# Optimization experiments

Measured on AMD Instinct MI355X. Metric: run time of the kernel, lower is better.

## Reference

```python
import jax, jax.numpy as jnp
import numpy as np
import math

D_MODEL = 256
D_STATE = 16
D_CONV = 4
EXPAND = 2
N_HEADS = 4
D_INNER = EXPAND * D_MODEL          # 512
DT_RANK = (D_MODEL + 15) // 16      # 16
B_SZ, SEQ = 4, 2048


def setup_inputs() -> dict:
    key = jax.random.key(0)
    ks = jax.random.split(key, 12)
    rn = lambda i, shp, sc=0.02: jax.random.normal(ks[i], shp, dtype=jnp.float32) * sc
    x = jax.random.normal(ks[0], (B_SZ, SEQ, D_MODEL), dtype=jnp.float32)
    return dict(
        x=x,
        ln_g=jnp.ones((D_MODEL,), jnp.float32),
        ln_b=jnp.zeros((D_MODEL,), jnp.float32),
        W_in=rn(1, (D_MODEL, 2 * D_INNER)),
        conv_w=rn(2, (D_INNER, D_CONV), 0.1),
        conv_b=jnp.zeros((D_INNER,), jnp.float32),
        W_xproj=rn(3, (D_INNER, DT_RANK + 2 * D_STATE)),
        W_dt=rn(4, (DT_RANK, D_INNER), 0.1),
        b_dt=jnp.full((D_INNER,), -4.6, jnp.float32),  # softplus ~ 0.01 init
        A_log=jnp.log(jnp.tile(jnp.arange(1, D_STATE + 1, dtype=jnp.float32), (D_INNER, 1))),
        Dp=jnp.ones((D_INNER,), jnp.float32),
        W_out_m=rn(5, (D_INNER, D_MODEL)),
        W_qkv=rn(6, (D_MODEL, 3 * D_MODEL)),
        b_qkv=jnp.zeros((3 * D_MODEL,), jnp.float32),
        W_o=rn(7, (D_MODEL, D_MODEL)),
        b_o=jnp.zeros((D_MODEL,), jnp.float32),
        W_gate=rn(8, (2 * D_MODEL, D_MODEL)),
        b_gate=jnp.zeros((D_MODEL,), jnp.float32),
    )


def _sssd_forward(x, ln_g, ln_b, W_in, conv_w, conv_b, W_xproj, W_dt, b_dt,
                  A_log, Dp, W_out_m, W_qkv, b_qkv, W_o, b_o, W_gate, b_gate):
    B, L, D = x.shape
    # LayerNorm
    mu = x.mean(-1, keepdims=True)
    var = x.var(-1, keepdims=True)
    xn = (x - mu) * jax.lax.rsqrt(var + 1e-5) * ln_g + ln_b

    # ---- Mamba branch ----
    xz = xn @ W_in                      # (B,L,2*D_INNER)
    xm, z = jnp.split(xz, 2, axis=-1)
    # causal depthwise conv1d (kernel D_CONV)
    xp = jnp.pad(xm, ((0, 0), (D_CONV - 1, 0), (0, 0)))
    xc = conv_b + sum(xp[:, k:k + L, :] * conv_w[:, k] for k in range(D_CONV))
    xc = jax.nn.silu(xc)
    dbl = xc @ W_xproj                  # (B,L,DT_RANK+2*D_STATE)
    dt_in = dbl[..., :DT_RANK]
    Bm = dbl[..., DT_RANK:DT_RANK + D_STATE]
    Cm = dbl[..., DT_RANK + D_STATE:]
    dt = jax.nn.softplus(dt_in @ W_dt + b_dt)   # (B,L,D_INNER)
    A = -jnp.exp(A_log)                 # (D_INNER, D_STATE)

    def step(h, inp):
        x_t, dt_t, B_t, C_t = inp       # (B,Din),(B,Din),(B,N),(B,N)
        dA = jnp.exp(dt_t[..., None] * A)               # (B,Din,N)
        h = dA * h + (dt_t * x_t)[..., None] * B_t[:, None, :]
        y = jnp.einsum('bdn,bn->bd', h, C_t)
        return h, y

    h0 = jnp.zeros((B, D_INNER, D_STATE), x.dtype)
    xs = (jnp.swapaxes(xc, 0, 1), jnp.swapaxes(dt, 0, 1),
          jnp.swapaxes(Bm, 0, 1), jnp.swapaxes(Cm, 0, 1))
    _, ys = jax.lax.scan(step, h0, xs)
    y = jnp.swapaxes(ys, 0, 1) + xc * Dp
    y = y * jax.nn.silu(z)
    ssm_out = y @ W_out_m               # (B,L,D)

    # ---- MHSA branch (eval: no dropout) ----
    hd = D // N_HEADS
    qkv = xn @ W_qkv + b_qkv
    q, k, v = jnp.split(qkv, 3, axis=-1)
    sh = lambda t: t.reshape(B, L, N_HEADS, hd).transpose(0, 2, 1, 3)
    q, k, v = sh(q), sh(k), sh(v)
    scores = jnp.einsum('bhqd,bhkd->bhqk', q, k) * (1.0 / math.sqrt(hd))
    attn = jax.nn.softmax(scores, axis=-1)
    o = jnp.einsum('bhqk,bhkd->bhqd', attn, v).transpose(0, 2, 1, 3).reshape(B, L, D)
    attn_out = o @ W_o + b_o

    # ---- sigmoid gate fusion ----
    gate = jax.nn.sigmoid(jnp.concatenate([ssm_out, attn_out], axis=-1) @ W_gate + b_gate)
    fused = gate * ssm_out + (1.0 - gate) * attn_out
    return x + fused


def reference(x, ln_g, ln_b, W_in, conv_w, conv_b, W_xproj, W_dt, b_dt,
              A_log, Dp, W_out_m, W_qkv, b_qkv, W_o, b_o, W_gate, b_gate):
    return _sssd_forward(x, ln_g, ln_b, W_in, conv_w, conv_b, W_xproj, W_dt, b_dt,
                         A_log, Dp, W_out_m, W_qkv, b_qkv, W_o, b_o, W_gate, b_gate)
```

## Files before the change

kernel.cpp:

```cpp
#include <hip/hip_runtime.h>
#include <math.h>

#define B_SZ 4
#define SEQ 2048
#define DM 256
#define DI 512
#define DS 16
#define DTR 16
#define NH 4
#define HD 64
#define T_TOK (B_SZ*SEQ)
#define NCH 64
#define CL (SEQ/NCH)
#define QSCALE 0.18033688f

typedef short bf16x8 __attribute__((ext_vector_type(8)));
typedef float f32x4  __attribute__((ext_vector_type(4)));
typedef float f32x16 __attribute__((ext_vector_type(16)));
typedef unsigned short u16;

__device__ __forceinline__ float sigmoidf_(float x){ return 1.f/(1.f+__expf(-x)); }
__device__ __forceinline__ u16 f2bf(float x){
  unsigned int u = __float_as_uint(x);
  u += 0x7fffu + ((u>>16)&1u);
  return (u16)(u>>16);
}
__device__ __forceinline__ float bf2f(u16 u){ return __uint_as_float(((unsigned)u)<<16); }
__device__ __forceinline__ unsigned cvt_pk_bf16(float lo, float hi){
  unsigned r;
  asm("v_cvt_pk_bf16_f32 %0, %1, %2" : "=v"(r) : "v"(lo), "v"(hi));
  return r;
}
__device__ __forceinline__ void permswap(unsigned &a, unsigned &b){
  asm volatile("v_permlane32_swap_b32 %0, %1" : "+v"(a), "+v"(b));
}
__device__ __forceinline__ float xor32f(float v){
  unsigned a = __float_as_uint(v), b = a;
  permswap(a, b);
  return __uint_as_float(a);
}

struct TcvtArgs {
  const float* src[6];
  u16* dst[6];
  int K[6];
  int Nvalid[6];
  int Npad[6];
};
__global__ __launch_bounds__(256) void tcvt_all(TcvtArgs a) {
  int wi = blockIdx.z;
  int K = a.K[wi], Nv = a.Nvalid[wi], Np = a.Npad[wi];
  int k0 = blockIdx.x*64, n0 = blockIdx.y*64;
  if (k0 >= K || n0 >= Np) return;
  __shared__ u16 tile[64][65];
  const float* src = a.src[wi];
  u16* dst = a.dst[wi];
  int tn = threadIdx.x & 63, tq = threadIdx.x >> 6;
#pragma unroll
  for (int j=0;j<16;++j){
    int kk = j*4 + tq;
    int n = n0 + tn;
    tile[tn][kk] = (n < Nv) ? f2bf(src[(size_t)(k0+kk)*Nv + n]) : (u16)0;
  }
  __syncthreads();
#pragma unroll
  for (int j=0;j<16;++j){
    int nn = j*4 + tq;
    dst[(size_t)(n0+nn)*K + k0 + tn] = tile[nn][tn];
  }
}

__global__ __launch_bounds__(256) void ln_kernel(const float* __restrict__ x,
    const float* __restrict__ g, const float* __restrict__ b,
    u16* __restrict__ xn_bf) {
  int wid = threadIdx.x >> 6;
  int lane = threadIdx.x & 63;
  int token = blockIdx.x*4 + wid;
  const float* xr = x + (size_t)token*DM;
  float4 v = *(const float4*)&xr[lane*4];
  float s  = v.x+v.y+v.z+v.w;
  float ss = v.x*v.x+v.y*v.y+v.z*v.z+v.w*v.w;
  for (int m=1;m<64;m<<=1){ s += __shfl_xor(s,m); ss += __shfl_xor(ss,m); }
  float mu  = s * (1.f/DM);
  float var = ss*(1.f/DM) - mu*mu;
  float rs  = rsqrtf(var + 1e-5f);
  float4 gv = *(const float4*)&g[lane*4];
  float4 bv = *(const float4*)&b[lane*4];
  uint2 o;
  o.x = cvt_pk_bf16((v.x-mu)*rs*gv.x + bv.x, (v.y-mu)*rs*gv.y + bv.y);
  o.y = cvt_pk_bf16((v.z-mu)*rs*gv.z + bv.z, (v.w-mu)*rs*gv.w + bv.w);
  *(uint2*)&xn_bf[(size_t)token*DM + lane*4] = o;
}

template<int ACT>
__global__ __launch_bounds__(256) void gemm_mfma(const u16* __restrict__ A,
    const u16* __restrict__ Wt, const float* __restrict__ bias,
    float* __restrict__ C, u16* __restrict__ Cbf, int K, int ldc, int nvalid,
    int qcols, float qscale, const float* __restrict__ xres,
    const float* __restrict__ cat2, u16* __restrict__ vTout) {
  __shared__ u16 lds[12288];
  int tid = threadIdx.x;
  int m0 = blockIdx.y*128, n0 = blockIdx.x*64;
  int w = tid>>6, l = tid&63, lq = l&15, lg = l>>4;
  int wm = w>>1, wn = w&1;
  f32x4 acc[4][2] = {};
  for (int k0 = 0; k0 < K; k0 += 64) {
#pragma unroll
    for (int i=0;i<4;++i){
      int gid = i*256 + tid;
      int row = gid>>3, g = gid&7;
      *(bf16x8*)&lds[row*64 + ((g ^ (row&7))*8)] =
          *(const bf16x8*)&A[(size_t)(m0+row)*K + k0 + g*8];
    }
#pragma unroll
    for (int i=0;i<2;++i){
      int gid = i*256 + tid;
      int row = gid>>3, g = gid&7;
      *(bf16x8*)&lds[8192 + row*64 + ((g ^ (row&7))*8)] =
          *(const bf16x8*)&Wt[(size_t)(n0+row)*K + k0 + g*8];
    }
    __syncthreads();
#pragma unroll
    for (int ks=0;ks<2;++ks){
      bf16x8 af[4], bfv[2];
#pragma unroll
      for (int mi=0;mi<4;++mi){
        int row = wm*64 + mi*16 + lq;
        af[mi] = *(bf16x8*)&lds[row*64 + (((ks*4+lg) ^ (row&7))*8)];
      }
#pragma unroll
      for (int nj=0;nj<2;++nj){
        int row = wn*32 + nj*16 + lq;
        bfv[nj] = *(bf16x8*)&lds[8192 + row*64 + (((ks*4+lg) ^ (row&7))*8)];
      }
#pragma unroll
      for (int mi=0;mi<4;++mi)
#pragma unroll
        for (int nj=0;nj<2;++nj)
          acc[mi][nj] = __builtin_amdgcn_mfma_f32_16x16x32_bf16(af[mi], bfv[nj], acc[mi][nj], 0,0,0);
    }
    __syncthreads();
  }
#pragma unroll
  for (int mi=0;mi<4;++mi){
#pragma unroll
    for (int nj=0;nj<2;++nj){
#pragma unroll
      for (int r=0;r<4;++r){
        int row = m0 + wm*64 + mi*16 + lg*4 + r;
        int col = n0 + wn*32 + nj*16 + lq;
        if (col < nvalid) {
          float v = acc[mi][nj][r];
          if (bias) v += bias[col];
          if (col < qcols) v *= qscale;
          if (ACT==2) {
            float g = sigmoidf_(v);
            float sv = cat2[(size_t)row*512 + col];
            float av = cat2[(size_t)row*512 + 256 + col];
            C[(size_t)row*256 + col] = xres[(size_t)row*256 + col] + g*sv + (1.f-g)*av;
          } else if (ACT==3) {
            Cbf[(size_t)row*ldc + col] = f2bf(v);
            if (col >= 512) {
              int bb = row>>11, ll = row&2047;
              int hh = (col-512)>>6, dd = (col-512)&63;
              vTout[(((size_t)(bb*4+hh))*64 + dd)*SEQ + ll] = f2bf(v);
            }
          } else {
            if (ACT==1) v = sigmoidf_(v);
            if (C)   C[(size_t)row*ldc + col] = v;
            if (Cbf) Cbf[(size_t)row*ldc + col] = f2bf(v);
          }
        }
      }
    }
  }
}

__global__ __launch_bounds__(256) void conv_kernel(const u16* __restrict__ xzb,
    const float* __restrict__ cw, const float* __restrict__ cb,
    u16* __restrict__ xc_bf) {
  int idx = blockIdx.x*256 + threadIdx.x;
  int d2 = (idx & 255)*2;
  int t = idx >> 8;
  int l = t & (SEQ-1);
  float acc0 = cb[d2], acc1 = cb[d2+1];
  float4 wA = *(const float4*)&cw[d2*4];
  float4 wB = *(const float4*)&cw[d2*4+4];
  const u16* base = xzb + (size_t)t*1024 + d2;
  ushort2 v;
  if (l>=3){ v = *(const ushort2*)&base[-3*1024]; acc0 += bf2f(v.x)*wA.x; acc1 += bf2f(v.y)*wB.x; }
  if (l>=2){ v = *(const ushort2*)&base[-2*1024]; acc0 += bf2f(v.x)*wA.y; acc1 += bf2f(v.y)*wB.y; }
  if (l>=1){ v = *(const ushort2*)&base[-1*1024]; acc0 += bf2f(v.x)*wA.z; acc1 += bf2f(v.y)*wB.z; }
  v = *(const ushort2*)&base[0];
  acc0 += bf2f(v.x)*wA.w; acc1 += bf2f(v.y)*wB.w;
  float r0 = acc0 * sigmoidf_(acc0);
  float r1 = acc1 * sigmoidf_(acc1);
  *(unsigned*)&xc_bf[(size_t)t*DI + d2] = cvt_pk_bf16(r0, r1);
}

__global__ __launch_bounds__(256) void dt_kernel(const float* __restrict__ dbl,
    const float* __restrict__ Wdt, const float* __restrict__ bdt,
    u16* __restrict__ dt) {
  __shared__ float sdbl[4][16];
  int wid = threadIdx.x>>6, lane = threadIdx.x&63;
  int token = blockIdx.x*4 + wid;
  if (lane < 16) sdbl[wid][lane] = dbl[(size_t)token*48 + lane];
  __syncthreads();
  float din[16];
#pragma unroll
  for (int k=0;k<16;++k) din[k] = sdbl[wid][k];
#pragma unroll
  for (int r=0;r<8;++r){
    int d = lane + r*64;
    float acc = bdt[d];
#pragma unroll
    for (int k=0;k<16;++k) acc += din[k]*Wdt[k*DI+d];
    float sp = (acc > 20.f) ? acc : log1pf(__expf(acc));
    dt[(size_t)token*DI+d] = f2bf(sp);
  }
}

__global__ __launch_bounds__(512) void scan_p1(const u16* __restrict__ xc_bf,
    const u16* __restrict__ dt, const float* __restrict__ dbl,
    const float* __restrict__ A_log, u16* __restrict__ Pws, u16* __restrict__ Hws) {
  __shared__ float sB[CL][16];
  int d = threadIdx.x;
  int bc = blockIdx.x;
  int b = bc >> 6, c = bc & 63;
  {
    int t = threadIdx.x >> 4, n = threadIdx.x & 15;
    sB[t][n] = dbl[((size_t)b*SEQ + c*CL + t)*48 + DTR + n];
  }
  __syncthreads();
  float An[16];
#pragma unroll
  for (int i=0;i<4;++i){
    float4 a = *(const float4*)&A_log[d*16 + i*4];
    An[i*4+0] = -__expf(a.x); An[i*4+1] = -__expf(a.y);
    An[i*4+2] = -__expf(a.z); An[i*4+3] = -__expf(a.w);
  }
  float h[16] = {};
  float P[16];
#pragma unroll
  for (int n=0;n<16;++n) P[n] = 1.f;
  size_t tok = (size_t)b*SEQ + c*CL;
  for (int t=0;t<CL;++t,++tok){
    float dtv = bf2f(dt[tok*DI+d]);
    float xcv = bf2f(xc_bf[tok*DI+d]);
    float u = dtv*xcv;
    float4 B0 = *(float4*)&sB[t][0];
    float4 B1 = *(float4*)&sB[t][4];
    float4 B2 = *(float4*)&sB[t][8];
    float4 B3 = *(float4*)&sB[t][12];
    float Bv[16] = {B0.x,B0.y,B0.z,B0.w,B1.x,B1.y,B1.z,B1.w,
                    B2.x,B2.y,B2.z,B2.w,B3.x,B3.y,B3.z,B3.w};
#pragma unroll
    for (int n=0;n<16;++n){
      float e = __expf(dtv*An[n]);
      P[n] *= e;
      h[n] = e*h[n] + u*Bv[n];
    }
  }
  size_t base = (((size_t)b*NCH + c)*DI + d)*16;
#pragma unroll
  for (int i=0;i<8;++i){
    *(unsigned*)&Pws[base + i*2] = cvt_pk_bf16(P[i*2], P[i*2+1]);
    *(unsigned*)&Hws[base + i*2] = cvt_pk_bf16(h[i*2], h[i*2+1]);
  }
}

__global__ __launch_bounds__(256) void scan_combine(const u16* __restrict__ Pws,
    const u16* __restrict__ Hws, u16* __restrict__ H0ws) {
  int gid = blockIdx.x*256 + threadIdx.x;
  int b  = gid >> 13;
  int dn = gid & 8191;
  float h0 = 0.f;
#pragma unroll 4
  for (int c=0;c<NCH;++c){
    size_t idx = ((size_t)(b*NCH+c)<<13) + dn;
    H0ws[idx] = f2bf(h0);
    h0 = bf2f(Pws[idx])*h0 + bf2f(Hws[idx]);
  }
}

__global__ __launch_bounds__(512) void scan_p2(const u16* __restrict__ xc_bf,
    const u16* __restrict__ dt, const float* __restrict__ dbl,
    const float* __restrict__ A_log, const float* __restrict__ Dp,
    const u16* __restrict__ xzb, const u16* __restrict__ H0ws,
    u16* __restrict__ ygate_bf) {
  __shared__ float sBC[CL][32];
  int d = threadIdx.x;
  int bc = blockIdx.x;
  int b = bc >> 6, c = bc & 63;
#pragma unroll
  for (int i=0;i<2;++i){
    int idx = i*512 + threadIdx.x;
    int t = idx >> 5, q = idx & 31;
    sBC[t][q] = dbl[((size_t)b*SEQ + c*CL + t)*48 + DTR + q];
  }
  __syncthreads();
  float An[16];
#pragma unroll
  for (int i=0;i<4;++i){
    float4 a = *(const float4*)&A_log[d*16 + i*4];
    An[i*4+0] = -__expf(a.x); An[i*4+1] = -__expf(a.y);
    An[i*4+2] = -__expf(a.z); An[i*4+3] = -__expf(a.w);
  }
  float Dd = Dp[d];
  float h[16];
  size_t base = (((size_t)b*NCH + c)*DI + d)*16;
  {
    bf16x8 h8a = *(const bf16x8*)&H0ws[base];
    bf16x8 h8b = *(const bf16x8*)&H0ws[base+8];
#pragma unroll
    for (int n=0;n<8;++n){ h[n] = bf2f((u16)h8a[n]); h[8+n] = bf2f((u16)h8b[n]); }
  }
  size_t tok = (size_t)b*SEQ + c*CL;
  for (int t=0;t<CL;++t,++tok){
    float dtv = bf2f(dt[tok*DI+d]);
    float xcv = bf2f(xc_bf[tok*DI+d]);
    float zv  = bf2f(xzb[tok*1024 + DI + d]);
    float u = dtv*xcv;
    float4 B0 = *(float4*)&sBC[t][0];
    float4 B1 = *(float4*)&sBC[t][4];
    float4 B2 = *(float4*)&sBC[t][8];
    float4 B3 = *(float4*)&sBC[t][12];
    float4 C0 = *(float4*)&sBC[t][16];
    float4 C1 = *(float4*)&sBC[t][20];
    float4 C2 = *(float4*)&sBC[t][24];
    float4 C3 = *(float4*)&sBC[t][28];
    float Bv[16] = {B0.x,B0.y,B0.z,B0.w,B1.x,B1.y,B1.z,B1.w,
                    B2.x,B2.y,B2.z,B2.w,B3.x,B3.y,B3.z,B3.w};
    float Cv[16] = {C0.x,C0.y,C0.z,C0.w,C1.x,C1.y,C1.z,C1.w,
                    C2.x,C2.y,C2.z,C2.w,C3.x,C3.y,C3.z,C3.w};
    float y = 0.f;
#pragma unroll
    for (int n=0;n<16;++n){
      float e = __expf(dtv*An[n]);
      h[n] = e*h[n] + u*Bv[n];
      y += h[n]*Cv[n];
    }
    y += xcv*Dd;
    ygate_bf[tok*DI + d] = f2bf(y * (zv*sigmoidf_(zv)));
  }
}

__global__ __launch_bounds__(256) void attn_mfma_kernel(const u16* __restrict__ qkvb,
    const u16* __restrict__ vT,
    u16* __restrict__ Opart, float* __restrict__ ml) {
  __shared__ u16 lds[8192];
  int H = blockIdx.x + 8*blockIdx.y + 128*(int)blockIdx.z;
  int cx = H & 7, kk = H >> 3;
  int xq = kk & 7;
  int G  = cx*8 + (kk >> 3);
  int bh = G & 15, s = G >> 4;
  int b = bh>>2, h = bh&3;
  int tid = threadIdx.x;
  int w = tid>>6, l = tid&63;
  int lo32 = l & 31;
  int hi = l >> 5;
  size_t bbase = (size_t)b*SEQ;
  size_t vbase = (size_t)bh*HD*SEQ;
  int q_base = xq*256 + w*64;

  bf16x8 qf[2][4];
#pragma unroll
  for (int qg=0; qg<2; ++qg)
#pragma unroll
    for (int dsl=0; dsl<4; ++dsl)
      qf[qg][dsl] = *(const bf16x8*)&qkvb[(bbase + q_base + qg*32 + lo32)*768 + h*HD + dsl*16 + hi*8];

  float m_[2] = {-1e30f,-1e30f}, l_[2] = {0.f,0.f};
  f32x16 oacc[2][2] = {};

  int srow = tid>>3, sg = tid&7;
  int kt0 = s*8;
  bf16x8 kreg[2], vreg[2];

#define LOADT(kt) { \
  kreg[0] = *(const bf16x8*)&qkvb[(bbase + (size_t)(kt)*64 + srow)*768 + 256 + h*HD + sg*8]; \
  kreg[1] = *(const bf16x8*)&qkvb[(bbase + (size_t)(kt)*64 + srow + 32)*768 + 256 + h*HD + sg*8]; \
  vreg[0] = *(const bf16x8*)&vT[vbase + (size_t)srow*SEQ + (kt)*64 + sg*8]; \
  vreg[1] = *(const bf16x8*)&vT[vbase + (size_t)(srow+32)*SEQ + (kt)*64 + sg*8]; }
#define STORET() { \
  *(bf16x8*)&lds[srow*64 + ((sg ^ (srow&7))*8)] = kreg[0]; \
  *(bf16x8*)&lds[(srow+32)*64 + ((sg ^ ((srow+32)&7))*8)] = kreg[1]; \
  *(bf16x8*)&lds[4096 + srow*64 + ((sg ^ (srow&7))*8)] = vreg[0]; \
  *(bf16x8*)&lds[4096 + (srow+32)*64 + ((sg ^ ((srow+32)&7))*8)] = vreg[1]; }
#define EXCH(X, Y, s_own, s_oth) { \
  unsigned xa = (X), yb = (Y); \
  permswap(xa, yb); \
  s_own = (l < 32) ? (X) : xa; \
  s_oth = (l < 32) ? yb : (Y); }

  LOADT(kt0);
  for (int it=0; it<8; ++it){
    __syncthreads();
    STORET();
    __syncthreads();
    if (it < 7) LOADT(kt0+it+1);

#pragma unroll
    for (int t32=0; t32<2; ++t32){
      int krow = t32*32 + lo32;
      bf16x8 kf[4];
#pragma unroll
      for (int dsl=0; dsl<4; ++dsl)
        kf[dsl] = *(bf16x8*)&lds[krow*64 + (((dsl*2 + hi) ^ (krow&7))*8)];

      bf16x8 pf[2][2];
#pragma unroll
      for (int qg=0; qg<2; ++qg){
        f32x16 sacc = {0,0,0,0,0,0,0,0,0,0,0,0,0,0,0,0};
#pragma unroll
        for (int dsl=0; dsl<4; ++dsl)
          sacc = __builtin_amdgcn_mfma_f32_32x32x16_bf16(kf[dsl], qf[qg][dsl], sacc, 0,0,0);

        float tm = sacc[0];
#pragma unroll
        for (int r=1;r<16;++r) tm = fmaxf(tm, sacc[r]);
        tm = fmaxf(tm, xor32f(tm));
        if (__any(tm - m_[qg] > 8.f)) {
          float mn = fmaxf(m_[qg], tm);
          float sc = exp2f(m_[qg] - mn);
          m_[qg] = mn;
          l_[qg] *= sc;
#pragma unroll
          for (int r=0;r<16;++r){ oacc[qg][0][r] *= sc; oacc[qg][1][r] *= sc; }
        }
        float p[16];
        float ps = 0.f;
#pragma unroll
        for (int r=0;r<16;++r){ p[r] = exp2f(sacc[r] - m_[qg]); ps += p[r]; }
        ps += xor32f(ps);
        l_[qg] += ps;

        unsigned A0 = cvt_pk_bf16(p[0],p[1]),  A1 = cvt_pk_bf16(p[2],p[3]);
        unsigned B0 = cvt_pk_bf16(p[4],p[5]),  B1 = cvt_pk_bf16(p[6],p[7]);
        unsigned C0 = cvt_pk_bf16(p[8],p[9]),  C1 = cvt_pk_bf16(p[10],p[11]);
        unsigned D0 = cvt_pk_bf16(p[12],p[13]),D1 = cvt_pk_bf16(p[14],p[15]);
        unsigned s0,s1,s2,s3,s4,s5,s6,s7;
        EXCH(A0,B0,s0,s2); EXCH(A1,B1,s1,s3);
        EXCH(C0,D0,s4,s6); EXCH(C1,D1,s5,s7);
        ((unsigned*)&pf[qg][0])[0]=s0; ((unsigned*)&pf[qg][0])[1]=s1;
        ((unsigned*)&pf[qg][0])[2]=s2; ((unsigned*)&pf[qg][0])[3]=s3;
        ((unsigned*)&pf[qg][1])[0]=s4; ((unsigned*)&pf[qg][1])[1]=s5;
        ((unsigned*)&pf[qg][1])[2]=s6; ((unsigned*)&pf[qg][1])[3]=s7;
      }

#pragma unroll
      for (int dtile=0; dtile<2; ++dtile){
        int vrow = dtile*32 + lo32;
        bf16x8 vf0 = *(bf16x8*)&lds[4096 + vrow*64 + (((t32*4 + 0 + hi) ^ (vrow&7))*8)];
        bf16x8 vf1 = *(bf16x8*)&lds[4096 + vrow*64 + (((t32*4 + 2 + hi) ^ (vrow&7))*8)];
        oacc[0][dtile] = __builtin_amdgcn_mfma_f32_32x32x16_bf16(vf0, pf[0][0], oacc[0][dtile], 0,0,0);
        oacc[0][dtile] = __builtin_amdgcn_mfma_f32_32x32x16_bf16(vf1, pf[0][1], oacc[0][dtile], 0,0,0);
        oacc[1][dtile] = __builtin_amdgcn_mfma_f32_32x32x16_bf16(vf0, pf[1][0], oacc[1][dtile], 0,0,0);
        oacc[1][dtile] = __builtin_amdgcn_mfma_f32_32x32x16_bf16(vf1, pf[1][1], oacc[1][dtile], 0,0,0);
      }
    }
  }
#undef LOADT
#undef STORET
#undef EXCH

  int sidx = bh*4 + s;
#pragma unroll
  for (int qg=0; qg<2; ++qg){
    size_t rb = ((size_t)sidx*SEQ + q_base + qg*32 + lo32)*64;
#pragma unroll
    for (int dtile=0; dtile<2; ++dtile){
#pragma unroll
      for (int rg=0; rg<4; ++rg){
        uint2 pk;
        pk.x = cvt_pk_bf16(oacc[qg][dtile][rg*4+0], oacc[qg][dtile][rg*4+1]);
        pk.y = cvt_pk_bf16(oacc[qg][dtile][rg*4+2], oacc[qg][dtile][rg*4+3]);
        *(uint2*)&Opart[rb + dtile*32 + rg*8 + 4*hi] = pk;
      }
    }
    if (l < 32){
      ml[((size_t)sidx*SEQ + q_base + qg*32 + lo32)*2    ] = m_[qg];
      ml[((size_t)sidx*SEQ + q_base + qg*32 + lo32)*2 + 1] = l_[qg];
    }
  }
}

__global__ __launch_bounds__(256) void attn_merge_kernel(const u16* __restrict__ Opart,
    const float* __restrict__ ml, u16* __restrict__ attn_bf) {
  int w = threadIdx.x>>6, lane = threadIdx.x&63;
  int R = blockIdx.x*4 + w;
  int bh = R>>11, q = R&2047;
  float m[4], lv[4];
#pragma unroll
  for (int s=0;s<4;++s){
    m[s]  = ml[((size_t)(bh*4+s)*SEQ + q)*2];
    lv[s] = ml[((size_t)(bh*4+s)*SEQ + q)*2 + 1];
  }
  float ms = fmaxf(fmaxf(m[0],m[1]),fmaxf(m[2],m[3]));
  float o = 0.f, lsum = 0.f;
#pragma unroll
  for (int s=0;s<4;++s){
    float wsc = exp2f(m[s]-ms);
    lsum += wsc*lv[s];
    o += wsc*bf2f(Opart[((size_t)(bh*4+s)*SEQ + q)*64 + lane]);
  }
  size_t token = (size_t)(bh>>2)*SEQ + q;
  attn_bf[token*DM + (bh&3)*HD + lane] = f2bf(o/lsum);
}

extern "C" void kernel_launch(void* const* d_in, const int* in_sizes, int n_in,
                              void* d_out, int out_size, void* d_ws, size_t ws_size,
                              hipStream_t stream) {
  const float* x      = (const float*)d_in[0];
  const float* ln_g   = (const float*)d_in[1];
  const float* ln_b   = (const float*)d_in[2];
  const float* W_in   = (const float*)d_in[3];
  const float* conv_w = (const float*)d_in[4];
  const float* conv_b = (const float*)d_in[5];
  const float* W_xproj= (const float*)d_in[6];
  const float* W_dt   = (const float*)d_in[7];
  const float* b_dt   = (const float*)d_in[8];
  const float* A_log  = (const float*)d_in[9];
  const float* Dp     = (const float*)d_in[10];
  const float* W_out_m= (const float*)d_in[11];
  const float* W_qkv  = (const float*)d_in[12];
  const float* b_qkv  = (const float*)d_in[13];
  const float* W_o    = (const float*)d_in[14];
  const float* b_o    = (const float*)d_in[15];
  const float* W_gate = (const float*)d_in[16];
  const float* b_gate = (const float*)d_in[17];
  float* out = (float*)d_out;

  float* ws = (float*)d_ws;
  u16*   xn_bf   = (u16*)(ws);
  u16*   xzb     = (u16*)(ws + 1048576);
  u16*   qkv_bf  = (u16*)(ws + 9437184);
  u16*   xc_bf   = (u16*)(ws + 12582912);
  float* dblb    = ws + 16777216;
  u16*   dtb     = (u16*)(ws + 17170432);
  u16*   ygate_bf= (u16*)(ws + 21364736);
  u16*   attn_bf = (u16*)(ws + 23461888);
  float* catb    = ws + 24510464;
  u16*   catb_bf = (u16*)(ws + 28704768);
  float* gateb   = ws + 30801920;
  u16*   Wt_all  = (u16*)(ws + 32899072);
  u16*   Opart = (u16*)(ws + 1048576);
  float* mlb   = (float*)xn_bf;
  u16*   vTb   = (u16*)gateb;
  u16*   Pws   = (u16*)catb;
  u16*   Hws   = (u16*)(catb + 1048576);
  u16*   H0ws  = (u16*)(catb + 2097152);

  u16* Wt_in   = Wt_all;
  u16* Wt_qkv  = Wt_all + 262144;
  u16* Wt_out  = Wt_all + 458752;
  u16* Wt_o    = Wt_all + 589824;
  u16* Wt_gate = Wt_all + 655360;
  u16* Wt_xp   = Wt_all + 786432;

  TcvtArgs ta;
  ta.src[0]=W_in;    ta.dst[0]=Wt_in;   ta.K[0]=256; ta.Nvalid[0]=1024; ta.Npad[0]=1024;
  ta.src[1]=W_qkv;   ta.dst[1]=Wt_qkv;  ta.K[1]=256; ta.Nvalid[1]=768;  ta.Npad[1]=768;
  ta.src[2]=W_out_m; ta.dst[2]=Wt_out;  ta.K[2]=512; ta.Nvalid[2]=256;  ta.Npad[2]=256;
  ta.src[3]=W_o;     ta.dst[3]=Wt_o;    ta.K[3]=256; ta.Nvalid[3]=256;  ta.Npad[3]=256;
  ta.src[4]=W_gate;  ta.dst[4]=Wt_gate; ta.K[4]=512; ta.Nvalid[4]=256;  ta.Npad[4]=256;
  ta.src[5]=W_xproj; ta.dst[5]=Wt_xp;   ta.K[5]=512; ta.Nvalid[5]=48;   ta.Npad[5]=64;
  tcvt_all<<<dim3(8,16,6), 256, 0, stream>>>(ta);

  ln_kernel<<<T_TOK/4, 256, 0, stream>>>(x, ln_g, ln_b, xn_bf);
  gemm_mfma<0><<<dim3(16,64), 256, 0, stream>>>(xn_bf, Wt_in, nullptr, nullptr, xzb, 256, 1024, 1024, 0, 1.f, nullptr, nullptr, nullptr);
  gemm_mfma<3><<<dim3(12,64), 256, 0, stream>>>(xn_bf, Wt_qkv, b_qkv, nullptr, qkv_bf, 256, 768, 768, 256, QSCALE, nullptr, nullptr, vTb);
  conv_kernel<<<T_TOK, 256, 0, stream>>>(xzb, conv_w, conv_b, xc_bf);
  gemm_mfma<0><<<dim3(1,64), 256, 0, stream>>>(xc_bf, Wt_xp, nullptr, dblb, nullptr, 512, 48, 48, 0, 1.f, nullptr, nullptr, nullptr);
  dt_kernel<<<T_TOK/4, 256, 0, stream>>>(dblb, W_dt, b_dt, dtb);
  scan_p1<<<B_SZ*NCH, 512, 0, stream>>>(xc_bf, dtb, dblb, A_log, Pws, Hws);
  scan_combine<<<128, 256, 0, stream>>>(Pws, Hws, H0ws);
  scan_p2<<<B_SZ*NCH, 512, 0, stream>>>(xc_bf, dtb, dblb, A_log, Dp, xzb, H0ws, ygate_bf);
  attn_mfma_kernel<<<dim3(8, 16, 4), 256, 0, stream>>>(qkv_bf, vTb, Opart, mlb);
  attn_merge_kernel<<<8192, 256, 0, stream>>>(Opart, mlb, attn_bf);
  gemm_mfma<0><<<dim3(4,64), 256, 0, stream>>>(ygate_bf, Wt_out, nullptr, catb, catb_bf, 512, 512, 256, 0, 1.f, nullptr, nullptr, nullptr);
  gemm_mfma<0><<<dim3(4,64), 256, 0, stream>>>(attn_bf, Wt_o, b_o, catb+256, catb_bf+256, 256, 512, 256, 0, 1.f, nullptr, nullptr, nullptr);
  gemm_mfma<2><<<dim3(4,64), 256, 0, stream>>>(catb_bf, Wt_gate, b_gate, out, nullptr, 512, 256, 256, 0, 1.f, x, catb, nullptr);
}
```

Measured before the change: 242.6 us.

## Fuse dt projection into scan passes and attention merge into Wo GEMM

Removes the separate dt_kernel and computes the dt projection plus softplus inline inside both scan passes, using the dt_in columns staged in shared memory. The dt intermediate buffer and its global round trip go away, but each pass now recomputes a 16-term dot product and a log1p/exp per element. The attention split-K merge kernel is also folded into the A-tile load of the output-projection GEMM through a new ACT==4 path. That path reads the four partial outputs and their max/sum stats directly, so attn_bf is no longer materialised. The price is extra ALU work in the serial scan loop and heavier, less coalesced loads in the GEMM prologue.

```diff
diff --git a/kernel.cpp b/kernel.cpp
--- a/kernel.cpp
+++ b/kernel.cpp
@@ -97,7 +97,8 @@
     const u16* __restrict__ Wt, const float* __restrict__ bias,
     float* __restrict__ C, u16* __restrict__ Cbf, int K, int ldc, int nvalid,
     int qcols, float qscale, const float* __restrict__ xres,
-    const float* __restrict__ cat2, u16* __restrict__ vTout) {
+    const float* __restrict__ cat2, u16* __restrict__ vTout,
+    const float* __restrict__ mlp) {
   __shared__ u16 lds[12288];
   int tid = threadIdx.x;
   int m0 = blockIdx.y*128, n0 = blockIdx.x*64;
@@ -105,12 +106,49 @@
   int wm = w>>1, wn = w&1;
   f32x4 acc[4][2] = {};
   for (int k0 = 0; k0 < K; k0 += 64) {
-#pragma unroll
-    for (int i=0;i<4;++i){
-      int gid = i*256 + tid;
-      int row = gid>>3, g = gid&7;
-      *(bf16x8*)&lds[row*64 + ((g ^ (row&7))*8)] =
-          *(const bf16x8*)&A[(size_t)(m0+row)*K + k0 + g*8];
+    if (ACT==4) {
+#pragma unroll
+      for (int i=0;i<4;++i){
+        int gid = i*256 + tid;
+        int row = gid>>3, g = gid&7;
+        int token = m0+row;
+        int bq = token>>11, q = token&2047;
+        int dcol = k0 + g*8;
+        int hh = dcol>>6, dd = dcol&63;
+        int bh4 = (bq*4+hh)*4;
+        float mm[4], lv[4];
+#pragma unroll
+        for (int s4=0;s4<4;++s4){
+          mm[s4] = mlp[((size_t)(bh4+s4)*SEQ+q)*2];
+          lv[s4] = mlp[((size_t)(bh4+s4)*SEQ+q)*2+1];
+        }
+        float ms = fmaxf(fmaxf(mm[0],mm[1]),fmaxf(mm[2],mm[3]));
+        float wsc[4]; float lsum=0.f;
+#pragma unroll
+        for (int s4=0;s4<4;++s4){ wsc[s4]=exp2f(mm[s4]-ms); lsum += wsc[s4]*lv[s4]; }
+        float inv = 1.f/lsum;
+        bf16x8 vpart[4];
+#pragma unroll
+        for (int s4=0;s4<4;++s4)
+          vpart[s4] = *(const bf16x8*)&A[(((size_t)(bh4+s4)*SEQ)+q)*64 + dd];
+        bf16x8 outv;
+#pragma unroll
+        for (int j=0;j<8;++j){
+          float o = 0.f;
+#pragma unroll
+          for (int s4=0;s4<4;++s4) o += wsc[s4]*bf2f((u16)vpart[s4][j]);
+          outv[j] = (short)f2bf(o*inv);
+        }
+        *(bf16x8*)&lds[row*64 + ((g ^ (row&7))*8)] = outv;
+      }
+    } else {
+#pragma unroll
+      for (int i=0;i<4;++i){
+        int gid = i*256 + tid;
+        int row = gid>>3, g = gid&7;
+        *(bf16x8*)&lds[row*64 + ((g ^ (row&7))*8)] =
+            *(const bf16x8*)&A[(size_t)(m0+row)*K + k0 + g*8];
+      }
     }
 #pragma unroll
     for (int i=0;i<2;++i){
@@ -198,40 +236,25 @@
   *(unsigned*)&xc_bf[(size_t)t*DI + d2] = cvt_pk_bf16(r0, r1);
 }
 
-__global__ __launch_bounds__(256) void dt_kernel(const float* __restrict__ dbl,
+__global__ __launch_bounds__(512) void scan_p1(const u16* __restrict__ xc_bf,
+    const float* __restrict__ dbl, const float* __restrict__ A_log,
     const float* __restrict__ Wdt, const float* __restrict__ bdt,
-    u16* __restrict__ dt) {
-  __shared__ float sdbl[4][16];
-  int wid = threadIdx.x>>6, lane = threadIdx.x&63;
-  int token = blockIdx.x*4 + wid;
-  if (lane < 16) sdbl[wid][lane] = dbl[(size_t)token*48 + lane];
-  __syncthreads();
-  float din[16];
-#pragma unroll
-  for (int k=0;k<16;++k) din[k] = sdbl[wid][k];
-#pragma unroll
-  for (int r=0;r<8;++r){
-    int d = lane + r*64;
-    float acc = bdt[d];
-#pragma unroll
-    for (int k=0;k<16;++k) acc += din[k]*Wdt[k*DI+d];
-    float sp = (acc > 20.f) ? acc : log1pf(__expf(acc));
-    dt[(size_t)token*DI+d] = f2bf(sp);
-  }
-}
-
-__global__ __launch_bounds__(512) void scan_p1(const u16* __restrict__ xc_bf,
-    const u16* __restrict__ dt, const float* __restrict__ dbl,
-    const float* __restrict__ A_log, u16* __restrict__ Pws, u16* __restrict__ Hws) {
-  __shared__ float sB[CL][16];
+    u16* __restrict__ Pws, u16* __restrict__ Hws) {
+  __shared__ float sB[CL][32];
   int d = threadIdx.x;
   int bc = blockIdx.x;
   int b = bc >> 6, c = bc & 63;
   {
     int t = threadIdx.x >> 4, n = threadIdx.x & 15;
-    sB[t][n] = dbl[((size_t)b*SEQ + c*CL + t)*48 + DTR + n];
+#pragma unroll
+    for (int i=0;i<2;++i)
+      sB[t][i*16+n] = dbl[((size_t)b*SEQ + c*CL + t)*48 + i*16 + n];
   }
   __syncthreads();
+  float wdt[16];
+#pragma unroll
+  for (int k=0;k<16;++k) wdt[k] = Wdt[k*DI + d];
+  float bdt_d = bdt[d];
   float An[16];
 #pragma unroll
   for (int i=0;i<4;++i){
@@ -245,13 +268,16 @@
   for (int n=0;n<16;++n) P[n] = 1.f;
   size_t tok = (size_t)b*SEQ + c*CL;
   for (int t=0;t<CL;++t,++tok){
-    float dtv = bf2f(dt[tok*DI+d]);
+    float dacc = bdt_d;
+#pragma unroll
+    for (int k=0;k<16;++k) dacc += sB[t][k]*wdt[k];
+    float dtv = (dacc > 20.f) ? dacc : log1pf(__expf(dacc));
     float xcv = bf2f(xc_bf[tok*DI+d]);
     float u = dtv*xcv;
-    float4 B0 = *(float4*)&sB[t][0];
-    float4 B1 = *(float4*)&sB[t][4];
-    float4 B2 = *(float4*)&sB[t][8];
-    float4 B3 = *(float4*)&sB[t][12];
+    float4 B0 = *(float4*)&sB[t][16];
+    float4 B1 = *(float4*)&sB[t][20];
+    float4 B2 = *(float4*)&sB[t][24];
+    float4 B3 = *(float4*)&sB[t][28];
     float Bv[16] = {B0.x,B0.y,B0.z,B0.w,B1.x,B1.y,B1.z,B1.w,
                     B2.x,B2.y,B2.z,B2.w,B3.x,B3.y,B3.z,B3.w};
 #pragma unroll
@@ -284,21 +310,25 @@
 }
 
 __global__ __launch_bounds__(512) void scan_p2(const u16* __restrict__ xc_bf,
-    const u16* __restrict__ dt, const float* __restrict__ dbl,
-    const float* __restrict__ A_log, const float* __restrict__ Dp,
-    const u16* __restrict__ xzb, const u16* __restrict__ H0ws,
-    u16* __restrict__ ygate_bf) {
-  __shared__ float sBC[CL][32];
+    const float* __restrict__ dbl, const float* __restrict__ A_log,
+    const float* __restrict__ Wdt, const float* __restrict__ bdt,
+    const float* __restrict__ Dp, const u16* __restrict__ xzb,
+    const u16* __restrict__ H0ws, u16* __restrict__ ygate_bf) {
+  __shared__ float sBC[CL][48];
   int d = threadIdx.x;
   int bc = blockIdx.x;
   int b = bc >> 6, c = bc & 63;
-#pragma unroll
-  for (int i=0;i<2;++i){
-    int idx = i*512 + threadIdx.x;
-    int t = idx >> 5, q = idx & 31;
-    sBC[t][q] = dbl[((size_t)b*SEQ + c*CL + t)*48 + DTR + q];
+  {
+    int t = threadIdx.x >> 4, n = threadIdx.x & 15;
+#pragma unroll
+    for (int i=0;i<3;++i)
+      sBC[t][i*16+n] = dbl[((size_t)b*SEQ + c*CL + t)*48 + i*16 + n];
   }
   __syncthreads();
+  float wdt[16];
+#pragma unroll
+  for (int k=0;k<16;++k) wdt[k] = Wdt[k*DI + d];
+  float bdt_d = bdt[d];
   float An[16];
 #pragma unroll
   for (int i=0;i<4;++i){
@@ -317,18 +347,21 @@
   }
   size_t tok = (size_t)b*SEQ + c*CL;
   for (int t=0;t<CL;++t,++tok){
-    float dtv = bf2f(dt[tok*DI+d]);
+    float dacc = bdt_d;
+#pragma unroll
+    for (int k=0;k<16;++k) dacc += sBC[t][k]*wdt[k];
+    float dtv = (dacc > 20.f) ? dacc : log1pf(__expf(dacc));
     float xcv = bf2f(xc_bf[tok*DI+d]);
     float zv  = bf2f(xzb[tok*1024 + DI + d]);
     float u = dtv*xcv;
-    float4 B0 = *(float4*)&sBC[t][0];
-    float4 B1 = *(float4*)&sBC[t][4];
-    float4 B2 = *(float4*)&sBC[t][8];
-    float4 B3 = *(float4*)&sBC[t][12];
-    float4 C0 = *(float4*)&sBC[t][16];
-    float4 C1 = *(float4*)&sBC[t][20];
-    float4 C2 = *(float4*)&sBC[t][24];
-    float4 C3 = *(float4*)&sBC[t][28];
+    float4 B0 = *(float4*)&sBC[t][16];
+    float4 B1 = *(float4*)&sBC[t][20];
+    float4 B2 = *(float4*)&sBC[t][24];
+    float4 B3 = *(float4*)&sBC[t][28];
+    float4 C0 = *(float4*)&sBC[t][32];
+    float4 C1 = *(float4*)&sBC[t][36];
+    float4 C2 = *(float4*)&sBC[t][40];
+    float4 C3 = *(float4*)&sBC[t][44];
     float Bv[16] = {B0.x,B0.y,B0.z,B0.w,B1.x,B1.y,B1.z,B1.w,
                     B2.x,B2.y,B2.z,B2.w,B3.x,B3.y,B3.z,B3.w};
     float Cv[16] = {C0.x,C0.y,C0.z,C0.w,C1.x,C1.y,C1.z,C1.w,
@@ -483,29 +516,6 @@
       ml[((size_t)sidx*SEQ + q_base + qg*32 + lo32)*2 + 1] = l_[qg];
     }
   }
-}
-
-__global__ __launch_bounds__(256) void attn_merge_kernel(const u16* __restrict__ Opart,
-    const float* __restrict__ ml, u16* __restrict__ attn_bf) {
-  int w = threadIdx.x>>6, lane = threadIdx.x&63;
-  int R = blockIdx.x*4 + w;
-  int bh = R>>11, q = R&2047;
-  float m[4], lv[4];
-#pragma unroll
-  for (int s=0;s<4;++s){
-    m[s]  = ml[((size_t)(bh*4+s)*SEQ + q)*2];
-    lv[s] = ml[((size_t)(bh*4+s)*SEQ + q)*2 + 1];
-  }
-  float ms = fmaxf(fmaxf(m[0],m[1]),fmaxf(m[2],m[3]));
-  float o = 0.f, lsum = 0.f;
-#pragma unroll
-  for (int s=0;s<4;++s){
-    float wsc = exp2f(m[s]-ms);
-    lsum += wsc*lv[s];
-    o += wsc*bf2f(Opart[((size_t)(bh*4+s)*SEQ + q)*64 + lane]);
-  }
-  size_t token = (size_t)(bh>>2)*SEQ + q;
-  attn_bf[token*DM + (bh&3)*HD + lane] = f2bf(o/lsum);
 }
 
 extern "C" void kernel_launch(void* const* d_in, const int* in_sizes, int n_in,
@@ -537,9 +547,7 @@
   u16*   qkv_bf  = (u16*)(ws + 9437184);
   u16*   xc_bf   = (u16*)(ws + 12582912);
   float* dblb    = ws + 16777216;
-  u16*   dtb     = (u16*)(ws + 17170432);
   u16*   ygate_bf= (u16*)(ws + 21364736);
-  u16*   attn_bf = (u16*)(ws + 23461888);
   float* catb    = ws + 24510464;
   u16*   catb_bf = (u16*)(ws + 28704768);
   float* gateb   = ws + 30801920;
@@ -568,17 +576,15 @@
   tcvt_all<<<dim3(8,16,6), 256, 0, stream>>>(ta);
 
   ln_kernel<<<T_TOK/4, 256, 0, stream>>>(x, ln_g, ln_b, xn_bf);
-  gemm_mfma<0><<<dim3(16,64), 256, 0, stream>>>(xn_bf, Wt_in, nullptr, nullptr, xzb, 256, 1024, 1024, 0, 1.f, nullptr, nullptr, nullptr);
-  gemm_mfma<3><<<dim3(12,64), 256, 0, stream>>>(xn_bf, Wt_qkv, b_qkv, nullptr, qkv_bf, 256, 768, 768, 256, QSCALE, nullptr, nullptr, vTb);
+  gemm_mfma<0><<<dim3(16,64), 256, 0, stream>>>(xn_bf, Wt_in, nullptr, nullptr, xzb, 256, 1024, 1024, 0, 1.f, nullptr, nullptr, nullptr, nullptr);
+  gemm_mfma<3><<<dim3(12,64), 256, 0, stream>>>(xn_bf, Wt_qkv, b_qkv, nullptr, qkv_bf, 256, 768, 768, 256, QSCALE, nullptr, nullptr, vTb, nullptr);
   conv_kernel<<<T_TOK, 256, 0, stream>>>(xzb, conv_w, conv_b, xc_bf);
-  gemm_mfma<0><<<dim3(1,64), 256, 0, stream>>>(xc_bf, Wt_xp, nullptr, dblb, nullptr, 512, 48, 48, 0, 1.f, nullptr, nullptr, nullptr);
-  dt_kernel<<<T_TOK/4, 256, 0, stream>>>(dblb, W_dt, b_dt, dtb);
-  scan_p1<<<B_SZ*NCH, 512, 0, stream>>>(xc_bf, dtb, dblb, A_log, Pws, Hws);
+  gemm_mfma<0><<<dim3(1,64), 256, 0, stream>>>(xc_bf, Wt_xp, nullptr, dblb, nullptr, 512, 48, 48, 0, 1.f, nullptr, nullptr, nullptr, nullptr);
+  scan_p1<<<B_SZ*NCH, 512, 0, stream>>>(xc_bf, dblb, A_log, W_dt, b_dt, Pws, Hws);
   scan_combine<<<128, 256, 0, stream>>>(Pws, Hws, H0ws);
-  scan_p2<<<B_SZ*NCH, 512, 0, stream>>>(xc_bf, dtb, dblb, A_log, Dp, xzb, H0ws, ygate_bf);
+  scan_p2<<<B_SZ*NCH, 512, 0, stream>>>(xc_bf, dblb, A_log, W_dt, b_dt, Dp, xzb, H0ws, ygate_bf);
   attn_mfma_kernel<<<dim3(8, 16, 4), 256, 0, stream>>>(qkv_bf, vTb, Opart, mlb);
-  attn_merge_kernel<<<8192, 256, 0, stream>>>(Opart, mlb, attn_bf);
-  gemm_mfma<0><<<dim3(4,64), 256, 0, stream>>>(ygate_bf, Wt_out, nullptr, catb, catb_bf, 512, 512, 256, 0, 1.f, nullptr, nullptr, nullptr);
-  gemm_mfma<0><<<dim3(4,64), 256, 0, stream>>>(attn_bf, Wt_o, b_o, catb+256, catb_bf+256, 256, 512, 256, 0, 1.f, nullptr, nullptr, nullptr);
-  gemm_mfma<2><<<dim3(4,64), 256, 0, stream>>>(catb_bf, Wt_gate, b_gate, out, nullptr, 512, 256, 256, 0, 1.f, x, catb, nullptr);
-}
+  gemm_mfma<0><<<dim3(4,64), 256, 0, stream>>>(ygate_bf, Wt_out, nullptr, catb, catb_bf, 512, 512, 256, 0, 1.f, nullptr, nullptr, nullptr, nullptr);
+  gemm_mfma<4><<<dim3(4,64), 256, 0, stream>>>(Opart, Wt_o, b_o, catb+256, catb_bf+256, 256, 512, 256, 0, 1.f, nullptr, nullptr, nullptr, mlb);
+  gemm_mfma<2><<<dim3(4,64), 256, 0, stream>>>(catb_bf, Wt_gate, b_gate, out, nullptr, 512, 256, 256, 0, 1.f, x, catb, nullptr, nullptr);
+}
```

After: 256.6 us. 1.06x slower.
